# Performance work log

Measured on AMD Instinct MI355X. Metric: run time of the kernel, lower is better.

Reference implementation:

```python
import jax, jax.numpy as jnp
import numpy as np

B, S, H, NH = 16, 512, 768, 12
HD = H // NH


def setup_inputs() -> dict:
    key = jax.random.key(0)
    ks = jax.random.split(key, 8)
    w = 0.02
    return {
        "x": jax.random.normal(ks[0], (B, S, H), jnp.float32),
        "key_padding_mask": jnp.zeros((B, S), jnp.bool_),
        "in_proj_w": jax.random.normal(ks[1], (3 * H, H), jnp.float32) * w,
        "in_proj_b": jnp.zeros((3 * H,), jnp.float32),
        "out_proj_w": jax.random.normal(ks[2], (H, H), jnp.float32) * w,
        "out_proj_b": jnp.zeros((H,), jnp.float32),
        "w1": jax.random.normal(ks[3], (4 * H, H), jnp.float32) * w,
        "b1": jnp.zeros((4 * H,), jnp.float32),
        "w2": jax.random.normal(ks[4], (H, 4 * H), jnp.float32) * w,
        "b2": jnp.zeros((H,), jnp.float32),
        "ln1_g": jnp.ones((H,), jnp.float32),
        "ln1_b": jnp.zeros((H,), jnp.float32),
        "ln2_g": jnp.ones((H,), jnp.float32),
        "ln2_b": jnp.zeros((H,), jnp.float32),
    }


def _layernorm(x, g, b, eps=1e-5):
    m = jnp.mean(x, axis=-1, keepdims=True)
    v = jnp.var(x, axis=-1, keepdims=True)
    return (x - m) / jnp.sqrt(v + eps) * g + b


def reference(x, key_padding_mask, in_proj_w, in_proj_b, out_proj_w, out_proj_b,
              w1, b1, w2, b2, ln1_g, ln1_b, ln2_g, ln2_b):
    b, s, h = x.shape
    # --- nn.MultiheadAttention (batch_first, need_weights, per-head weights) ---
    qkv = x @ in_proj_w.T + in_proj_b                      # [B,S,3H]
    q, k, v = jnp.split(qkv, 3, axis=-1)
    q = q.reshape(b, s, NH, HD).transpose(0, 2, 1, 3)      # [B,NH,S,HD]
    k = k.reshape(b, s, NH, HD).transpose(0, 2, 1, 3)
    v = v.reshape(b, s, NH, HD).transpose(0, 2, 1, 3)
    scale = 1.0 / np.sqrt(HD).astype(np.float32)
    scores = jnp.einsum('bhqd,bhkd->bhqk', q * scale, k)   # [B,NH,S,S]
    scores = jnp.where(key_padding_mask[:, None, None, :], -jnp.inf, scores)
    attn_weights = jax.nn.softmax(scores, axis=-1)         # returned per-head
    attn_out = jnp.einsum('bhqk,bhkd->bhqd', attn_weights, v)
    attn_out = attn_out.transpose(0, 2, 1, 3).reshape(b, s, h)
    attn_out = attn_out @ out_proj_w.T + out_proj_b
    # --- residual + LN, FFN + residual + LN (dropout is identity in eval) ---
    x = _layernorm(x + attn_out, ln1_g, ln1_b)
    ffn = jax.nn.gelu(x @ w1.T + b1, approximate=False) @ w2.T + b2
    x = _layernorm(x + ffn, ln2_g, ln2_b)
    return x, attn_weights
```

## Files before the change

### kernel.cpp

```cpp
#include <hip/hip_runtime.h>
#include <hip/hip_bf16.h>
#include <math.h>

typedef __bf16 bf16;
typedef __attribute__((ext_vector_type(8))) __bf16 bf16x8;
typedef __attribute__((ext_vector_type(4))) __bf16 bf16x4;
typedef __attribute__((ext_vector_type(4))) float f32x4;

#define B_  16
#define S_  512
#define H_  768
#define NH_ 12
#define HD_ 64
#define A_  (B_*S_)

__device__ __forceinline__ void gload_lds16(const void* g, void* l) {
  __builtin_amdgcn_global_load_lds((const __attribute__((address_space(1))) void*)g,
                                   (__attribute__((address_space(3))) void*)l, 16, 0, 0);
}

__device__ __forceinline__ float gelu_fast(float v) {
  const float u = 1.5957691216057308f * v * (1.0f + 0.044715f * v * v);
  return v / (1.0f + __expf(-u));
}

template<int EPI, int SPLIT>
__global__ __launch_bounds__(512, 4) void k_gemm_db(
    const bf16* __restrict__ Amat, const bf16* __restrict__ Bt,
    const float* __restrict__ bias, const bf16* __restrict__ resB,
    bf16* __restrict__ outB, float* __restrict__ outF,
    bf16* __restrict__ outQ, bf16* __restrict__ outK, bf16* __restrict__ outVT,
    int M, int N, int Kstride)
{
  constexpr int BN_ = 192, NFRAG = 3, SLOT_E = 8192 + BN_*64, WN = 48;
  __shared__ __align__(16) bf16 LDS[2 * SLOT_E];
  const int tid = threadIdx.x;
  const int w = tid >> 6, l = tid & 63;
  const int lr = l & 15, hi = l >> 4;
  const int wm = w >> 2, wn = w & 3;

  const int nbx = N / BN_;
  const int cpx = gridDim.x >> 3;
  const int sw  = (blockIdx.x & 7) * cpx + (blockIdx.x >> 3);
  const int tile  = sw >> SPLIT;
  const int slice = sw & ((1 << SPLIT) - 1);
  const int by = tile / nbx, bx = tile - by * nbx;
  const int row0 = by * 128, col0 = bx * BN_;
  const int Klen = Kstride >> SPLIT;
  const int koff = slice * Klen;
  const int NT = Klen / 64;

  auto stage = [&](int t, int u) {
    bf16* slot = LDS + (t & 1) * SLOT_E;
    if (u < 2) {
      const int fc = u*512 + tid;
      const int r = fc >> 3, s = fc & 7;
      const int gs = s ^ (r & 7);
      gload_lds16(Amat + (size_t)(row0 + r)*Kstride + koff + t*64 + gs*8,
                  slot + (size_t)fc*8 - (size_t)l*8);
    } else {
      const int fc = (u-2)*512 + tid;
      const int r = fc >> 3, s = fc & 7;
      const int gs = s ^ (r & 7);
      gload_lds16(Bt + (size_t)(col0 + r)*Kstride + koff + t*64 + gs*8,
                  slot + 8192 + (size_t)fc*8 - (size_t)l*8);
    }
  };

  f32x4 acc[4][NFRAG] = {};

#pragma unroll
  for (int u = 0; u < 5; ++u) stage(0, u);
  asm volatile("s_waitcnt vmcnt(0)" ::: "memory");
  __builtin_amdgcn_s_barrier();

  for (int t = 0; t < NT; ++t) {
    const bf16* slot = LDS + (t & 1) * SLOT_E;
    const bool pre = (t + 1 < NT);

    bf16x8 af[4], bfr[NFRAG];
#pragma unroll
    for (int m = 0; m < 4; ++m) {
      const int r = wm*64 + m*16 + lr;
      af[m] = *(const bf16x8*)(slot + r*64 + (hi ^ (r & 7))*8);
    }
#pragma unroll
    for (int n = 0; n < NFRAG; ++n) {
      const int r = wn*WN + n*16 + lr;
      bfr[n] = *(const bf16x8*)(slot + 8192 + r*64 + (hi ^ (r & 7))*8);
    }
    if (pre) { stage(t+1, 0); stage(t+1, 1); stage(t+1, 2); }
    asm volatile("s_waitcnt lgkmcnt(0)" ::: "memory");
    __builtin_amdgcn_sched_barrier(0);
    __builtin_amdgcn_s_setprio(1);
#pragma unroll
    for (int m = 0; m < 4; ++m)
#pragma unroll
      for (int n = 0; n < NFRAG; ++n)
        acc[m][n] = __builtin_amdgcn_mfma_f32_16x16x32_bf16(af[m], bfr[n], acc[m][n], 0, 0, 0);
    __builtin_amdgcn_s_setprio(0);

#pragma unroll
    for (int m = 0; m < 4; ++m) {
      const int r = wm*64 + m*16 + lr;
      af[m] = *(const bf16x8*)(slot + r*64 + ((4 + hi) ^ (r & 7))*8);
    }
#pragma unroll
    for (int n = 0; n < NFRAG; ++n) {
      const int r = wn*WN + n*16 + lr;
      bfr[n] = *(const bf16x8*)(slot + 8192 + r*64 + ((4 + hi) ^ (r & 7))*8);
    }
    if (pre) { stage(t+1, 3); stage(t+1, 4); }
    asm volatile("s_waitcnt lgkmcnt(0)" ::: "memory");
    __builtin_amdgcn_sched_barrier(0);
    __builtin_amdgcn_s_setprio(1);
#pragma unroll
    for (int m = 0; m < 4; ++m)
#pragma unroll
      for (int n = 0; n < NFRAG; ++n)
        acc[m][n] = __builtin_amdgcn_mfma_f32_16x16x32_bf16(af[m], bfr[n], acc[m][n], 0, 0, 0);
    __builtin_amdgcn_s_setprio(0);

    if (t < NT - 1) {
      asm volatile("s_waitcnt vmcnt(0)" ::: "memory");
      __builtin_amdgcn_s_barrier();
    }
  }

#pragma unroll
  for (int m = 0; m < 4; ++m) {
#pragma unroll
    for (int n = 0; n < NFRAG; ++n) {
#pragma unroll
      for (int i = 0; i < 4; ++i) {
        const int row = row0 + wm*64 + m*16 + hi*4 + i;
        const int col = col0 + wn*WN + n*16 + lr;
        if constexpr (EPI == 5) {
          __builtin_nontemporal_store(acc[m][n][i],
              outF + (size_t)slice*M*N + (size_t)row*N + col);
        } else if constexpr (EPI == 2) {
          float v = acc[m][n][i] + bias[col];
          outB[(size_t)row*N + col] = (bf16)gelu_fast(v);
        } else if constexpr (EPI == 4) {
          float v = acc[m][n][i] + bias[col];
          v += (float)resB[(size_t)row*N + col];
          outB[(size_t)row*N + col] = (bf16)v;
        } else {
          float v = acc[m][n][i] + bias[col];
          const int b = row >> 9, s = row & 511;
          const int which = col / H_;
          const int hcol = col - which * H_;
          const int h = hcol >> 6, d = hcol & 63;
          const size_t bh = (size_t)b * NH_ + h;
          if (which == 0)      outQ[(bh*S_ + s)*HD_ + d] = (bf16)v;
          else if (which == 1) outK[(bh*S_ + s)*HD_ + d] = (bf16)v;
          else                 outVT[(bh*HD_ + d)*S_ + s] = (bf16)v;
        }
      }
    }
  }
}

__global__ __launch_bounds__(256) void k_attn_fused(
    const bf16* __restrict__ Qm, const bf16* __restrict__ Km, const bf16* __restrict__ VT,
    const unsigned char* __restrict__ mask, float* __restrict__ P, bf16* __restrict__ AO)
{
  __shared__ __align__(16) bf16 KVs[512*64];
  const int tid = threadIdx.x, w = tid >> 6, l = tid & 63;
  const int lr = l & 15, hi = l >> 4;
  const int cpx = gridDim.x >> 3;
  const int sw  = (blockIdx.x & 7) * cpx + (blockIdx.x >> 3);
  const int bh = sw >> 3, qt = sw & 7;
  const int b = bh / NH_, h = bh - b * NH_;
  const int swz = (lr & 7) << 4;

  const bf16* Kg = Km + (size_t)bh * S_ * HD_;
#pragma unroll
  for (int rnd = 0; rnd < 16; ++rnd) {
    const int c = rnd*256 + tid;
    const int row = c >> 3, col16 = (c & 7) ^ (row & 7);
    gload_lds16(Kg + row*HD_ + col16*8, KVs + (rnd*4 + w)*512);
  }
  const bf16* qrow_g = Qm + (size_t)bh * S_ * HD_ + (size_t)(qt*64 + w*16 + lr) * HD_;
  bf16x8 qf0 = *(const bf16x8*)(qrow_g + hi*8);
  bf16x8 qf1 = *(const bf16x8*)(qrow_g + 32 + hi*8);
  __syncthreads();

  f32x4 acc[32];
#pragma unroll
  for (int ct = 0; ct < 32; ++ct) acc[ct] = f32x4{0.f,0.f,0.f,0.f};
#pragma unroll
  for (int ct = 0; ct < 32; ++ct) {
    const char* kb = (const char*)(KVs + (ct*16 + lr)*64);
    bf16x8 a0 = *(const bf16x8*)(kb + ((hi*16) ^ swz));
    bf16x8 a1 = *(const bf16x8*)(kb + ((64 + hi*16) ^ swz));
    acc[ct] = __builtin_amdgcn_mfma_f32_16x16x32_bf16(a0, qf0, acc[ct], 0, 0, 0);
    acc[ct] = __builtin_amdgcn_mfma_f32_16x16x32_bf16(a1, qf1, acc[ct], 0, 0, 0);
  }
  __syncthreads();

  const bf16* Vg = VT + (size_t)bh * HD_ * S_;
#pragma unroll
  for (int rnd = 0; rnd < 16; ++rnd) {
    const int c = rnd*256 + tid;
    const int row = c >> 6, col16 = (c & 63) ^ (row & 7);
    gload_lds16(Vg + row*S_ + col16*8, KVs + (rnd*4 + w)*512);
  }

  const unsigned char* mrow = mask + b * S_;
  float mx = -1e30f;
#pragma unroll
  for (int ct = 0; ct < 32; ++ct) {
    const unsigned mk4 = *(const unsigned*)(mrow + ct*16 + hi*4);
#pragma unroll
    for (int i = 0; i < 4; ++i) {
      float v = acc[ct][i] * 0.125f;
      if ((mk4 >> (8*i)) & 0xff) v = -1e30f;
      acc[ct][i] = v;
      mx = fmaxf(mx, v);
    }
  }
  mx = fmaxf(mx, __shfl_xor(mx, 16));
  mx = fmaxf(mx, __shfl_xor(mx, 32));
  float sum = 0.f;
#pragma unroll
  for (int ct = 0; ct < 32; ++ct)
#pragma unroll
    for (int i = 0; i < 4; ++i) { float e = __expf(acc[ct][i] - mx); acc[ct][i] = e; sum += e; }
  sum += __shfl_xor(sum, 16);
  sum += __shfl_xor(sum, 32);
  const float inv = 1.f / sum;

  float* prow = P + ((size_t)bh*S_ + (size_t)qt*64 + w*16 + lr) * S_;
#pragma unroll
  for (int ct = 0; ct < 32; ++ct) {
#pragma unroll
    for (int i = 0; i < 4; ++i) acc[ct][i] *= inv;
    __builtin_nontemporal_store(acc[ct], (f32x4*)(prow + ct*16 + hi*4));
  }
  __syncthreads();

  f32x4 o[4] = {};
#pragma unroll
  for (int c = 0; c < 16; ++c) {
    bf16x8 pa;
#pragma unroll
    for (int i = 0; i < 4; ++i) { pa[i] = (bf16)acc[2*c][i]; pa[4+i] = (bf16)acc[2*c+1][i]; }
    const int cb0 = (64*c + 8*hi) ^ swz;
    const int cb1 = (64*c + 32 + 8*hi) ^ swz;
#pragma unroll
    for (int nt = 0; nt < 4; ++nt) {
      const char* vb = (const char*)(KVs + (nt*16 + lr)*512);
      bf16x4 v0 = *(const bf16x4*)(vb + cb0);
      bf16x4 v1 = *(const bf16x4*)(vb + cb1);
      bf16x8 vf = {v0[0],v0[1],v0[2],v0[3], v1[0],v1[1],v1[2],v1[3]};
      o[nt] = __builtin_amdgcn_mfma_f32_16x16x32_bf16(pa, vf, o[nt], 0, 0, 0);
    }
  }

  bf16* aorow = AO + ((size_t)(b*S_ + qt*64 + w*16))*H_ + h*HD_;
#pragma unroll
  for (int nt = 0; nt < 4; ++nt)
#pragma unroll
    for (int i = 0; i < 4; ++i)
      aorow[(size_t)(hi*4 + i)*H_ + nt*16 + lr] = (bf16)o[nt][i];
}

__global__ __launch_bounds__(256) void k_layernorm(
    const bf16* __restrict__ X, const float* __restrict__ g, const float* __restrict__ bta,
    bf16* __restrict__ outB)
{
  const int w = threadIdx.x >> 6, l = threadIdx.x & 63;
  const int row = blockIdx.x * 4 + w;
  const bf16* x = X + (size_t)row * H_;
  float v[12]; float s = 0.f, ss = 0.f;
#pragma unroll
  for (int j = 0; j < 3; ++j) {
    bf16x4 b4 = *(const bf16x4*)(x + l*4 + j*256);
#pragma unroll
    for (int e = 0; e < 4; ++e) {
      const float f = (float)b4[e];
      v[j*4 + e] = f; s += f; ss += f*f;
    }
  }
#pragma unroll
  for (int d = 1; d < 64; d <<= 1) { s += __shfl_xor(s, d); ss += __shfl_xor(ss, d); }
  const float mean = s * (1.f / H_);
  const float var  = ss * (1.f / H_) - mean * mean;
  const float inv  = rsqrtf(var + 1e-5f);
#pragma unroll
  for (int j = 0; j < 3; ++j) {
    const int c = l*4 + j*256;
    const float4 gv = *(const float4*)(g + c);
    const float4 bv = *(const float4*)(bta + c);
    bf16x4 o;
    o[0] = (bf16)((v[j*4+0] - mean)*inv*gv.x + bv.x);
    o[1] = (bf16)((v[j*4+1] - mean)*inv*gv.y + bv.y);
    o[2] = (bf16)((v[j*4+2] - mean)*inv*gv.z + bv.z);
    o[3] = (bf16)((v[j*4+3] - mean)*inv*gv.w + bv.w);
    *(bf16x4*)(outB + (size_t)row*H_ + c) = o;
  }
}

__global__ __launch_bounds__(256) void k_ln_ffn2(
    const float* __restrict__ p0, const float* __restrict__ p1,
    const float* __restrict__ b2, const bf16* __restrict__ res,
    const float* __restrict__ g, const float* __restrict__ bta,
    float* __restrict__ xout)
{
  const int w = threadIdx.x >> 6, l = threadIdx.x & 63;
  const int row = blockIdx.x * 4 + w;
  const size_t base = (size_t)row * H_;
  float v[12]; float s = 0.f, ss = 0.f;
#pragma unroll
  for (int j = 0; j < 3; ++j) {
    const int c = l*4 + j*256;
    const float4 a0 = *(const float4*)(p0 + base + c);
    const float4 a1 = *(const float4*)(p1 + base + c);
    const float4 bb = *(const float4*)(b2 + c);
    bf16x4 r4 = *(const bf16x4*)(res + base + c);
    v[j*4+0] = a0.x + a1.x + bb.x + (float)r4[0];
    v[j*4+1] = a0.y + a1.y + bb.y + (float)r4[1];
    v[j*4+2] = a0.z + a1.z + bb.z + (float)r4[2];
    v[j*4+3] = a0.w + a1.w + bb.w + (float)r4[3];
#pragma unroll
    for (int e = 0; e < 4; ++e) { s += v[j*4+e]; ss += v[j*4+e]*v[j*4+e]; }
  }
#pragma unroll
  for (int d = 1; d < 64; d <<= 1) { s += __shfl_xor(s, d); ss += __shfl_xor(ss, d); }
  const float mean = s * (1.f / H_);
  const float var  = ss * (1.f / H_) - mean * mean;
  const float inv  = rsqrtf(var + 1e-5f);
#pragma unroll
  for (int j = 0; j < 3; ++j) {
    const int c = l*4 + j*256;
    const float4 gv = *(const float4*)(g + c);
    const float4 bv = *(const float4*)(bta + c);
    f32x4 y;
    y[0] = (v[j*4+0] - mean)*inv*gv.x + bv.x;
    y[1] = (v[j*4+1] - mean)*inv*gv.y + bv.y;
    y[2] = (v[j*4+2] - mean)*inv*gv.z + bv.z;
    y[3] = (v[j*4+3] - mean)*inv*gv.w + bv.w;
    __builtin_nontemporal_store(y, (f32x4*)(xout + base + c));
  }
}

#define NB0 (A_*H_/1024)
#define NB1 (3*H_*H_/1024)
#define NB2 (H_*H_/1024)
#define NB3 (4*H_*H_/1024)
#define NB4 (4*H_*H_/1024)
__global__ void k_conv_all(
    const float* __restrict__ s0, bf16* __restrict__ d0,
    const float* __restrict__ s1, bf16* __restrict__ d1,
    const float* __restrict__ s2, bf16* __restrict__ d2,
    const float* __restrict__ s3, bf16* __restrict__ d3,
    const float* __restrict__ s4, bf16* __restrict__ d4)
{
  int b = blockIdx.x;
  const float* src; bf16* dst;
  if      (b < NB0)                   { src = s0; dst = d0; }
  else if ((b -= NB0) < NB1)          { src = s1; dst = d1; }
  else if ((b -= NB1) < NB2)          { src = s2; dst = d2; }
  else if ((b -= NB2) < NB3)          { src = s3; dst = d3; }
  else    { b -= NB3;                   src = s4; dst = d4; }
  const int i = (b * 256 + threadIdx.x) * 4;
  const float4 vv = *(const float4*)(src + i);
  bf16x4 o; o[0]=(bf16)vv.x; o[1]=(bf16)vv.y; o[2]=(bf16)vv.z; o[3]=(bf16)vv.w;
  *(bf16x4*)(dst + i) = o;
}

extern "C" void kernel_launch(void* const* d_in, const int* in_sizes, int n_in,
                              void* d_out, int out_size, void* d_ws, size_t ws_size,
                              hipStream_t stream) {
  const float* x      = (const float*)d_in[0];
  const unsigned char* mask = (const unsigned char*)d_in[1];
  const float* w_qkv  = (const float*)d_in[2];
  const float* b_qkv  = (const float*)d_in[3];
  const float* w_out  = (const float*)d_in[4];
  const float* b_out  = (const float*)d_in[5];
  const float* w1     = (const float*)d_in[6];
  const float* b1     = (const float*)d_in[7];
  const float* w2     = (const float*)d_in[8];
  const float* b2     = (const float*)d_in[9];
  const float* ln1g   = (const float*)d_in[10];
  const float* ln1b   = (const float*)d_in[11];
  const float* ln2g   = (const float*)d_in[12];
  const float* ln2b   = (const float*)d_in[13];

  float* xout = (float*)d_out;
  float* P    = xout + (size_t)A_ * H_;

  char* ws = (char*)d_ws;
  size_t off = 0;
  auto alloc = [&](size_t bytes) { char* p = ws + off; off += (bytes + 255) & ~255ull; return p; };

  bf16* xb   = (bf16*)alloc((size_t)A_*H_*2);
  bf16* wqkv = (bf16*)alloc((size_t)3*H_*H_*2);
  bf16* wo   = (bf16*)alloc((size_t)H_*H_*2);
  bf16* w1b  = (bf16*)alloc((size_t)4*H_*H_*2);
  bf16* w2b  = (bf16*)alloc((size_t)4*H_*H_*2);
  char* qreg = alloc((size_t)A_*H_*2*4);
  bf16* q  = (bf16*)qreg;
  bf16* kb = q  + (size_t)A_*H_;
  bf16* vt = kb + (size_t)A_*H_;
  bf16* ao = vt + (size_t)A_*H_;
  bf16* hbuf = q;
  bf16* y1b = (bf16*)alloc((size_t)A_*H_*2);
  bf16* x1b = (bf16*)alloc((size_t)A_*H_*2);
  float* part = (float*)alloc((size_t)2*A_*H_*4);

  k_conv_all<<<NB0+NB1+NB2+NB3+NB4, 256, 0, stream>>>(
      x, xb, w_qkv, wqkv, w_out, wo, w1, w1b, w2, w2b);

  k_gemm_db<0,0><<<(A_/128)*(3*H_/192), 512, 0, stream>>>(xb, wqkv, b_qkv, nullptr,
      nullptr, nullptr, q, kb, vt, A_, 3*H_, H_);
  k_attn_fused<<<B_*NH_*8, 256, 0, stream>>>(q, kb, vt, mask, P, ao);
  k_gemm_db<4,0><<<(A_/128)*(H_/192), 512, 0, stream>>>(ao, wo, b_out, xb,
      y1b, nullptr, nullptr, nullptr, nullptr, A_, H_, H_);
  k_layernorm<<<A_/4, 256, 0, stream>>>(y1b, ln1g, ln1b, x1b);
  k_gemm_db<2,0><<<(A_/128)*(4*H_/192), 512, 0, stream>>>(x1b, w1b, b1, nullptr,
      hbuf, nullptr, nullptr, nullptr, nullptr, A_, 4*H_, H_);
  k_gemm_db<5,1><<<(A_/128)*(H_/192)*2, 512, 0, stream>>>(hbuf, w2b, nullptr, nullptr,
      nullptr, part, nullptr, nullptr, nullptr, A_, H_, 4*H_);
  k_ln_ffn2<<<A_/4, 256, 0, stream>>>(part, part + (size_t)A_*H_, b2, x1b,
      ln2g, ln2b, xout);
}
```

Measured before the change: 292.2 us.

## Add triple-buffered 128x256 GEMM kernel for QKV and FFN1 projections

Adds a new GEMM kernel with a 128x256 output tile, a K-step of 32, and a three-slot LDS ring buffer using direct global-to-LDS loads with an XOR swizzle. Prefetch runs two stages ahead, and it raises wave priority around the MFMA block. The QKV projection and the FFN1+GELU GEMM switch to this kernel, and their epilogues are removed from the old double-buffered kernel. The aim is to hide load latency better and get more reuse from the larger N tile. The cost is fewer blocks and possibly different occupancy.

```diff
diff --git a/kernel.cpp b/kernel.cpp
--- a/kernel.cpp
+++ b/kernel.cpp
@@ -24,12 +24,117 @@
   return v / (1.0f + __expf(-u));
 }
 
+template<int EPI>
+__global__ __launch_bounds__(512, 4) void k_gemm_c3(
+    const bf16* __restrict__ Amat, const bf16* __restrict__ Bt,
+    const float* __restrict__ bias,
+    bf16* __restrict__ outB,
+    bf16* __restrict__ outQ, bf16* __restrict__ outK, bf16* __restrict__ outVT,
+    int M, int N, int K)
+{
+  constexpr int SLOT_E = 128*32 + 256*32;
+  __shared__ __align__(16) bf16 LDS[3 * SLOT_E];
+  const int tid = threadIdx.x;
+  const int w = tid >> 6, l = tid & 63;
+  const int lr = l & 15, hi = l >> 4;
+  const int wm = w >> 2, wn = w & 3;
+
+  const int nbx = N >> 8;
+  const int cpx = gridDim.x >> 3;
+  const int sw  = (blockIdx.x & 7) * cpx + (blockIdx.x >> 3);
+  const int by = sw / nbx, bx = sw - by * nbx;
+  const int row0 = by * 128, col0 = bx * 256;
+  const int NT = K >> 5;
+
+  auto stage = [&](int t, int u) {
+    bf16* slot = LDS + (t % 3) * SLOT_E;
+    if (u == 0) {
+      const int fc = tid;
+      const int r = fc >> 2, s = fc & 3;
+      const int gs = s ^ (r & 3);
+      gload_lds16(Amat + (size_t)(row0 + r)*K + t*32 + gs*8,
+                  slot + (size_t)fc*8 - (size_t)l*8);
+    } else {
+      const int fc = (u-1)*512 + tid;
+      const int r = fc >> 2, s = fc & 3;
+      const int gs = s ^ (r & 3);
+      gload_lds16(Bt + (size_t)(col0 + r)*K + t*32 + gs*8,
+                  slot + 4096 + (size_t)fc*8 - (size_t)l*8);
+    }
+  };
+
+  f32x4 acc[4][4] = {};
+
+#pragma unroll
+  for (int u = 0; u < 3; ++u) stage(0, u);
+#pragma unroll
+  for (int u = 0; u < 3; ++u) stage(1, u);
+  asm volatile("s_waitcnt vmcnt(3)" ::: "memory");
+  __builtin_amdgcn_s_barrier();
+
+  for (int t = 0; t < NT; ++t) {
+    const bf16* slot = LDS + (t % 3) * SLOT_E;
+
+    bf16x8 af[4], bfr[4];
+#pragma unroll
+    for (int m = 0; m < 4; ++m) {
+      const int r = wm*64 + m*16 + lr;
+      af[m] = *(const bf16x8*)(slot + r*32 + ((hi ^ (r & 3))*8));
+    }
+#pragma unroll
+    for (int n = 0; n < 4; ++n) {
+      const int r = wn*64 + n*16 + lr;
+      bfr[n] = *(const bf16x8*)(slot + 4096 + r*32 + ((hi ^ (r & 3))*8));
+    }
+    if (t + 2 < NT) { stage(t+2, 0); stage(t+2, 1); stage(t+2, 2); }
+    asm volatile("s_waitcnt lgkmcnt(0)" ::: "memory");
+    __builtin_amdgcn_sched_barrier(0);
+    __builtin_amdgcn_s_setprio(1);
+#pragma unroll
+    for (int m = 0; m < 4; ++m)
+#pragma unroll
+      for (int n = 0; n < 4; ++n)
+        acc[m][n] = __builtin_amdgcn_mfma_f32_16x16x32_bf16(af[m], bfr[n], acc[m][n], 0, 0, 0);
+    __builtin_amdgcn_s_setprio(0);
+
+    if (t < NT - 1) {
+      if (t + 2 < NT) asm volatile("s_waitcnt vmcnt(3)" ::: "memory");
+      else            asm volatile("s_waitcnt vmcnt(0)" ::: "memory");
+      __builtin_amdgcn_s_barrier();
+    }
+  }
+
+#pragma unroll
+  for (int m = 0; m < 4; ++m) {
+#pragma unroll
+    for (int n = 0; n < 4; ++n) {
+#pragma unroll
+      for (int i = 0; i < 4; ++i) {
+        const int row = row0 + wm*64 + m*16 + hi*4 + i;
+        const int col = col0 + wn*64 + n*16 + lr;
+        float v = acc[m][n][i] + bias[col];
+        if constexpr (EPI == 2) {
+          outB[(size_t)row*N + col] = (bf16)gelu_fast(v);
+        } else {
+          const int b = row >> 9, s = row & 511;
+          const int which = col / H_;
+          const int hcol = col - which * H_;
+          const int h = hcol >> 6, d = hcol & 63;
+          const size_t bh = (size_t)b * NH_ + h;
+          if (which == 0)      outQ[(bh*S_ + s)*HD_ + d] = (bf16)v;
+          else if (which == 1) outK[(bh*S_ + s)*HD_ + d] = (bf16)v;
+          else                 outVT[(bh*HD_ + d)*S_ + s] = (bf16)v;
+        }
+      }
+    }
+  }
+}
+
 template<int EPI, int SPLIT>
 __global__ __launch_bounds__(512, 4) void k_gemm_db(
     const bf16* __restrict__ Amat, const bf16* __restrict__ Bt,
     const float* __restrict__ bias, const bf16* __restrict__ resB,
     bf16* __restrict__ outB, float* __restrict__ outF,
-    bf16* __restrict__ outQ, bf16* __restrict__ outK, bf16* __restrict__ outVT,
     int M, int N, int Kstride)
 {
   constexpr int BN_ = 192, NFRAG = 3, SLOT_E = 8192 + BN_*64, WN = 48;
@@ -138,23 +243,10 @@
         if constexpr (EPI == 5) {
           __builtin_nontemporal_store(acc[m][n][i],
               outF + (size_t)slice*M*N + (size_t)row*N + col);
-        } else if constexpr (EPI == 2) {
-          float v = acc[m][n][i] + bias[col];
-          outB[(size_t)row*N + col] = (bf16)gelu_fast(v);
-        } else if constexpr (EPI == 4) {
+        } else {
           float v = acc[m][n][i] + bias[col];
           v += (float)resB[(size_t)row*N + col];
           outB[(size_t)row*N + col] = (bf16)v;
-        } else {
-          float v = acc[m][n][i] + bias[col];
-          const int b = row >> 9, s = row & 511;
-          const int which = col / H_;
-          const int hcol = col - which * H_;
-          const int h = hcol >> 6, d = hcol & 63;
-          const size_t bh = (size_t)b * NH_ + h;
-          if (which == 0)      outQ[(bh*S_ + s)*HD_ + d] = (bf16)v;
-          else if (which == 1) outK[(bh*S_ + s)*HD_ + d] = (bf16)v;
-          else                 outVT[(bh*HD_ + d)*S_ + s] = (bf16)v;
         }
       }
     }
@@ -413,16 +505,16 @@
   k_conv_all<<<NB0+NB1+NB2+NB3+NB4, 256, 0, stream>>>(
       x, xb, w_qkv, wqkv, w_out, wo, w1, w1b, w2, w2b);
 
-  k_gemm_db<0,0><<<(A_/128)*(3*H_/192), 512, 0, stream>>>(xb, wqkv, b_qkv, nullptr,
-      nullptr, nullptr, q, kb, vt, A_, 3*H_, H_);
+  k_gemm_c3<0><<<(A_/128)*(3*H_/256), 512, 0, stream>>>(xb, wqkv, b_qkv,
+      nullptr, q, kb, vt, A_, 3*H_, H_);
   k_attn_fused<<<B_*NH_*8, 256, 0, stream>>>(q, kb, vt, mask, P, ao);
   k_gemm_db<4,0><<<(A_/128)*(H_/192), 512, 0, stream>>>(ao, wo, b_out, xb,
-      y1b, nullptr, nullptr, nullptr, nullptr, A_, H_, H_);
+      y1b, nullptr, A_, H_, H_);
   k_layernorm<<<A_/4, 256, 0, stream>>>(y1b, ln1g, ln1b, x1b);
-  k_gemm_db<2,0><<<(A_/128)*(4*H_/192), 512, 0, stream>>>(x1b, w1b, b1, nullptr,
-      hbuf, nullptr, nullptr, nullptr, nullptr, A_, 4*H_, H_);
+  k_gemm_c3<2><<<(A_/128)*(4*H_/256), 512, 0, stream>>>(x1b, w1b, b1,
+      hbuf, nullptr, nullptr, nullptr, A_, 4*H_, H_);
   k_gemm_db<5,1><<<(A_/128)*(H_/192)*2, 512, 0, stream>>>(hbuf, w2b, nullptr, nullptr,
-      nullptr, part, nullptr, nullptr, nullptr, A_, H_, 4*H_);
+      nullptr, part, A_, H_, 4*H_);
   k_ln_ffn2<<<A_/4, 256, 0, stream>>>(part, part + (size_t)A_*H_, b2, x1b,
       ln2g, ln2b, xout);
 }
```

Result: slower. 306.4 us (+4.9%).
